# Kernel optimization log

Hardware: AMD Instinct MI355X
Metric: run time of the kernel (lower is better)

## Reference

```python
import math
import jax, jax.numpy as jnp
import numpy as np

B, S, H, M, E = 4, 4096, 1024, 1024, 16
CAPACITY_FACTOR = 2.0
ROUTE_SCALE = 1.0


def setup_inputs() -> dict:
    key = jax.random.key(0)
    ks = jax.random.split(key, 8)
    return {
        "hidden_states": jax.random.normal(ks[0], (B, S, H), dtype=jnp.float32),
        "hidden_states_unmodulated": jax.random.normal(ks[1], (B, S, H), dtype=jnp.float32),
        "timestep": jax.random.normal(ks[2], (B, H), dtype=jnp.float32),
        "gate_w": jax.random.normal(ks[3], (2 * H, E), dtype=jnp.float32) * 0.02,
        "gate_up_proj": jax.random.normal(ks[4], (E, H, 2 * M), dtype=jnp.float32) * 0.02,
        "down_proj": jax.random.normal(ks[5], (E, M, H), dtype=jnp.float32) * 0.02,
        "shared_gate_up_w": jax.random.normal(ks[6], (H, 2 * M), dtype=jnp.float32) * 0.02,
        "shared_down_w": jax.random.normal(ks[7], (M, H), dtype=jnp.float32) * 0.02,
    }


def reference(hidden_states, hidden_states_unmodulated, timestep, gate_w,
              gate_up_proj, down_proj, shared_gate_up_w, shared_down_w):
    b, s, h = hidden_states.shape
    e = gate_up_proj.shape[0]
    capacity = max(1, math.ceil(CAPACITY_FACTOR * s / e))  # static per shapes

    # --- router ---
    t = jnp.broadcast_to(timestep[:, None, :], (b, s, h))
    router_input = jnp.concatenate([t, hidden_states_unmodulated], axis=-1)  # [b,s,2h]
    logits = router_input @ gate_w                                           # [b,s,e]
    scores = jax.nn.sigmoid(logits.astype(jnp.float32)).astype(logits.dtype)
    affinity = jnp.swapaxes(scores, 1, 2)                                    # [b,e,s]

    # --- expert-choice top-k ---
    gating, top_idx = jax.lax.top_k(affinity, capacity)                      # [b,e,cap]
    offsets = (jnp.arange(b) * s)[:, None, None]
    gidx = jnp.swapaxes(offsets + top_idx, 0, 1).reshape(-1)                 # [e*b*cap]
    gflat = jnp.swapaxes(gating, 0, 1).reshape(-1)

    # normalize per-token scores over experts that picked the token
    sums = jnp.zeros(b * s, dtype=gflat.dtype).at[gidx].add(gflat)
    gflat = gflat / (sums[gidx] + 1e-12) * ROUTE_SCALE

    # --- dispatch + grouped SwiGLU experts ---
    x_flat = hidden_states.reshape(b * s, h)
    routed = x_flat[gidx].reshape(e, b * capacity, h)
    gu = jnp.einsum('eth,ehf->etf', routed, gate_up_proj)                    # [e,t,2m]
    g, u = jnp.split(gu, 2, axis=-1)
    expert_out = jnp.einsum('etm,emh->eth', jax.nn.silu(g) * u, down_proj)
    expert_out = expert_out.reshape(e * b * capacity, h)
    expert_out = (expert_out.astype(jnp.float32) *
                  gflat.astype(jnp.float32)[:, None]).astype(hidden_states.dtype)

    # --- shared expert (SwiGLUProj order: hidden * silu(gate)) ---
    hgu = hidden_states @ shared_gate_up_w                                   # [b,s,2m]
    hs_, hg = jnp.split(hgu, 2, axis=-1)
    shared = (hs_ * jax.nn.silu(hg)) @ shared_down_w                         # [b,s,h]

    # --- scatter combine ---
    out = shared.reshape(b * s, h).at[gidx].add(expert_out)
    return out.reshape(b, s, h)
```

## Files before the change

### kernel.cpp

```cpp
#include <hip/hip_runtime.h>
#include <math.h>

#define Bb 4
#define Ss 4096
#define Hh 1024
#define Mm 1024
#define Ee 16
#define CAPk 512

typedef unsigned short u16;
typedef __attribute__((ext_vector_type(8))) short short8;
typedef __attribute__((ext_vector_type(4))) float floatx4;
typedef __attribute__((ext_vector_type(4))) unsigned short ushort4v;

__device__ __forceinline__ float silu_f(float x) {
    return x / (1.0f + expf(-x));
}

__device__ __forceinline__ u16 f2b(float x) {
    union { float f; unsigned u; } v; v.f = x;
    unsigned r = (v.u + 0x7fffu + ((v.u >> 16) & 1u)) >> 16;
    return (u16)r;
}

__device__ __forceinline__ void gl_lds16(const void* g, void* l) {
    __builtin_amdgcn_global_load_lds((const __attribute__((address_space(1))) void*)g,
                                     (__attribute__((address_space(3))) void*)l, 16, 0, 0);
}


__global__ __launch_bounds__(256)
void conv_router(const float* __restrict__ hidden, u16* __restrict__ Xb,
                 const float* __restrict__ hsu,
                 const float* __restrict__ gate_w,
                 const float* __restrict__ timestep,
                 float* __restrict__ scores) {
    const int t = threadIdx.x;
    if (blockIdx.x >= 256) {
        int i = ((blockIdx.x - 256) * 256 + t) * 4;
        float4 v = *(const float4*)(hidden + i);
        ushort4v o = { f2b(v.x), f2b(v.y), f2b(v.z), f2b(v.w) };
        *(ushort4v*)(Xb + i) = o;
        return;
    }
    __shared__ float Xs[64 * 64];
    __shared__ float Gs[64 * 16];
    const int rbid = blockIdx.x;
    const int row0 = rbid * 64;
    const int b = row0 >> 12;
    const int wave = t >> 6, lane = t & 63;
    const int e0 = wave * 4;
    const float* gw2 = gate_w + (size_t)Hh * Ee;

    float tl0 = 0.f, tl1 = 0.f, tl2 = 0.f, tl3 = 0.f;
    {
        const float* tsrow = timestep + (size_t)b * Hh;
#pragma unroll
        for (int j = 0; j < 16; ++j) {
            int h = lane + 64 * j;
            float tv = tsrow[h];
            const float* gw = gate_w + (size_t)h * Ee + e0;
            tl0 += tv * gw[0]; tl1 += tv * gw[1]; tl2 += tv * gw[2]; tl3 += tv * gw[3];
        }
#pragma unroll
        for (int off = 32; off; off >>= 1) {
            tl0 += __shfl_xor(tl0, off); tl1 += __shfl_xor(tl1, off);
            tl2 += __shfl_xor(tl2, off); tl3 += __shfl_xor(tl3, off);
        }
    }

    float acc0 = 0.f, acc1 = 0.f, acc2 = 0.f, acc3 = 0.f;

    for (int k0 = 0; k0 < Hh; k0 += 64) {
        __syncthreads();
#pragma unroll
        for (int r = 0; r < 4; ++r) {
            int tok = r * 16 + (t >> 4);
            int cslot = t & 15;
            int g = cslot ^ (tok & 15);
            const float* src = hsu + (size_t)(row0 + tok) * Hh + k0 + g * 4;
            char* dst = (char*)Xs + r * 4096 + wave * 1024;
            gl_lds16(src, dst);
        }
        {
            const float* src = gw2 + (size_t)k0 * Ee + t * 4;
            char* dst = (char*)Gs + wave * 1024;
            gl_lds16(src, dst);
        }
        __syncthreads();
#pragma unroll
        for (int kk = 0; kk < 64; kk += 4) {
            int slot = (kk >> 2) ^ (lane & 15);
            float4 a = *(const float4*)&Xs[lane * 64 + slot * 4];
            float4 g0 = *(const float4*)&Gs[(kk + 0) * Ee + e0];
            float4 g1 = *(const float4*)&Gs[(kk + 1) * Ee + e0];
            float4 g2 = *(const float4*)&Gs[(kk + 2) * Ee + e0];
            float4 g3 = *(const float4*)&Gs[(kk + 3) * Ee + e0];
            acc0 += a.x * g0.x; acc0 += a.y * g1.x; acc0 += a.z * g2.x; acc0 += a.w * g3.x;
            acc1 += a.x * g0.y; acc1 += a.y * g1.y; acc1 += a.z * g2.y; acc1 += a.w * g3.y;
            acc2 += a.x * g0.z; acc2 += a.y * g1.z; acc2 += a.z * g2.z; acc2 += a.w * g3.z;
            acc3 += a.x * g0.w; acc3 += a.y * g1.w; acc3 += a.z * g2.w; acc3 += a.w * g3.w;
        }
    }
    const int s = (row0 + lane) & (Ss - 1);
    float l0 = acc0 + tl0;
    float l1 = acc1 + tl1;
    float l2 = acc2 + tl2;
    float l3 = acc3 + tl3;
    scores[((size_t)(b * Ee + e0 + 0)) * Ss + s] = 1.f / (1.f + expf(-l0));
    scores[((size_t)(b * Ee + e0 + 1)) * Ss + s] = 1.f / (1.f + expf(-l1));
    scores[((size_t)(b * Ee + e0 + 2)) * Ss + s] = 1.f / (1.f + expf(-l2));
    scores[((size_t)(b * Ee + e0 + 3)) * Ss + s] = 1.f / (1.f + expf(-l3));
}

__global__ __launch_bounds__(1024)
void topk_kernel(const float* __restrict__ scores,
                 int* __restrict__ rank) {
    const int be = blockIdx.x;
    const float* sc = scores + (size_t)be * Ss;
    int* rk = rank + (size_t)be * Ss;
    const int t = threadIdx.x;
    const int lane = t & 63, w = t >> 6;
    __shared__ unsigned hist[256];
    __shared__ unsigned wtot[16];
    __shared__ unsigned sh_prefix;
    __shared__ int sh_need;
    __shared__ unsigned cnt_gt;

#pragma unroll
    for (int i = 0; i < 4; ++i) rk[t * 4 + i] = -1;

    unsigned vu[4];
#pragma unroll
    for (int i = 0; i < 4; ++i) vu[i] = __float_as_uint(sc[t * 4 + i]);

    unsigned prefix = 0;
    int need = CAPk;
    for (int pass = 0; pass < 4; ++pass) {
        const int shift = 24 - 8 * pass;
        if (t < 256) hist[t] = 0;
        __syncthreads();
#pragma unroll
        for (int i = 0; i < 4; ++i) {
            unsigned u = vu[i];
            bool ok = (pass == 0) || ((u >> (shift + 8)) == prefix);
            if (ok) atomicAdd(&hist[(u >> shift) & 255u], 1u);
        }
        __syncthreads();
        unsigned hval = (t < 256) ? hist[t] : 0u;
        unsigned s = hval;
#pragma unroll
        for (int d = 1; d < 64; d <<= 1) {
            unsigned o = __shfl_down(s, d);
            if (lane + d < 64) s += o;
        }
        if (lane == 0 && w < 4) wtot[w] = s;
        __syncthreads();
        if (t < 256) {
#pragma unroll
            for (int w2 = 0; w2 < 4; ++w2)
                if (w2 > w) s += wtot[w2];
            unsigned Snext = s - hval;
            if (s >= (unsigned)need && Snext < (unsigned)need) {
                sh_prefix = (prefix << 8) | (unsigned)t;
                sh_need = need - (int)Snext;
            }
        }
        __syncthreads();
        prefix = sh_prefix;
        need = sh_need;
        __syncthreads();
    }
    const unsigned T = prefix;
    const int need_eq = need;
    const unsigned ngt = (unsigned)(CAPk - need_eq);

    int myeq = 0;
#pragma unroll
    for (int i = 0; i < 4; ++i) myeq += (vu[i] == T) ? 1 : 0;
    unsigned e = (unsigned)myeq;
#pragma unroll
    for (int d = 1; d < 64; d <<= 1) {
        unsigned o = __shfl_up(e, d);
        if (lane >= d) e += o;
    }
    if (lane == 63) wtot[w] = e;
    if (t == 0) cnt_gt = 0;
    __syncthreads();
    unsigned eqr = e - (unsigned)myeq;
#pragma unroll
    for (int w2 = 0; w2 < 16; ++w2)
        if (w2 < w) eqr += wtot[w2];
#pragma unroll
    for (int i = 0; i < 4; ++i) {
        unsigned u = vu[i];
        int s = t * 4 + i;
        if (u > T) {
            unsigned slot = atomicAdd(&cnt_gt, 1u);
            rk[s] = (int)slot;
        } else if (u == T) {
            if ((int)eqr < need_eq) {
                rk[s] = (int)(ngt + eqr);
            }
            eqr++;
        }
    }
}

__global__ __launch_bounds__(256)
void route_build(const float* __restrict__ scores, const int* __restrict__ rank,
                 int* __restrict__ slot_token, float* __restrict__ slot_w,
                 int* __restrict__ cnt, int* __restrict__ inv) {
    const int token = blockIdx.x * 256 + threadIdx.x;
    const int b = token >> 12, s = token & (Ss - 1);
    int rr[16];
    float gg[16];
    float sum = 0.f;
#pragma unroll
    for (int e = 0; e < 16; ++e) {
        size_t idx = (size_t)(b * Ee + e) * Ss + s;
        int r = rank[idx];
        rr[e] = r;
        float g = (r >= 0) ? scores[idx] : 0.f;
        gg[e] = g;
        sum += g;
    }
    int pos = 0;
#pragma unroll
    for (int e = 0; e < 16; ++e) {
        if (rr[e] >= 0) {
            float wv = gg[e] / (sum + 1e-12f);
            int o = (e * Bb + b) * CAPk + rr[e];
            slot_token[o] = token;
            slot_w[o] = wv;
            inv[token * 16 + pos] = o;
            ++pos;
        }
    }
    cnt[token] = pos;
}

__global__ __launch_bounds__(256)
void combine_kernel(const int* __restrict__ cnt, const int* __restrict__ inv,
                    const float* __restrict__ eo, float* __restrict__ out) {
    const int token = blockIdx.x;
    const int k = cnt[token];
    if (k == 0) return;
    const int col = threadIdx.x * 4;
    const size_t rowoff = (size_t)token * 1024 + col;
    float4 acc = *(const float4*)(out + rowoff);
    for (int j = 0; j < k; ++j) {
        int slot = inv[token * 16 + j];
        float4 v = *(const float4*)(eo + (size_t)slot * 1024 + col);
        acc.x += v.x; acc.y += v.y; acc.z += v.z; acc.w += v.w;
    }
    *(float4*)(out + rowoff) = acc;
}


__device__ __forceinline__ void tpose_body(const float* __restrict__ Ws, u16* __restrict__ Wd,
                                           int N, int n0, int k0, float tile[64][65], int t) {
    int lr = t >> 4, lc = (t & 15) * 4;
#pragma unroll
    for (int i = 0; i < 4; ++i) {
        float4 v = *(const float4*)&Ws[(size_t)(k0 + lr + i * 16) * N + n0 + lc];
        tile[lr + i * 16][lc + 0] = v.x;
        tile[lr + i * 16][lc + 1] = v.y;
        tile[lr + i * 16][lc + 2] = v.z;
        tile[lr + i * 16][lc + 3] = v.w;
    }
    __syncthreads();
    int on = t >> 2;
    int ok0 = (t & 3) * 16;
    u16 buf[16];
#pragma unroll
    for (int j = 0; j < 16; ++j) buf[j] = f2b(tile[ok0 + j][on]);
    u16* dp = &Wd[(size_t)(n0 + on) * 1024 + k0 + ok0];
    *(short8*)(dp) = *(short8*)&buf[0];
    *(short8*)(dp + 8) = *(short8*)&buf[8];
}

__global__ __launch_bounds__(256)
void transpose_bf16(const float* __restrict__ W, u16* __restrict__ Wt,
                    int N, size_t zsrc, size_t zdst) {
    __shared__ float tile[64][65];
    int n0 = blockIdx.x * 64, k0 = blockIdx.y * 64, z = blockIdx.z;
    tpose_body(W + (size_t)z * zsrc, Wt + (size_t)z * zdst, N, n0, k0, tile, threadIdx.x);
}

__global__ __launch_bounds__(256)
void transpose_all(const float* __restrict__ gate_up, const float* __restrict__ down,
                   const float* __restrict__ sh_gu, const float* __restrict__ sh_dn,
                   u16* __restrict__ Wt1r, u16* __restrict__ Wt2r,
                   u16* __restrict__ Wt1s, u16* __restrict__ Wt2s) {
    __shared__ float tile[64][65];
    const int id = blockIdx.x;
    const float* Ws; u16* Wd; int N, n0, k0;
    if (id < 8192) {
        int z = id >> 9, r = id & 511;
        n0 = (r & 31) * 64; k0 = (r >> 5) * 64; N = 2048;
        Ws = gate_up + (size_t)z * 2097152; Wd = Wt1r + (size_t)z * 2097152;
    } else if (id < 12288) {
        int i2 = id - 8192; int z = i2 >> 8, r = i2 & 255;
        n0 = (r & 15) * 64; k0 = (r >> 4) * 64; N = 1024;
        Ws = down + (size_t)z * 1048576; Wd = Wt2r + (size_t)z * 1048576;
    } else if (id < 12800) {
        int r = id - 12288;
        n0 = (r & 31) * 64; k0 = (r >> 5) * 64; N = 2048;
        Ws = sh_gu; Wd = Wt1s;
    } else {
        int r = id - 12800;
        n0 = (r & 15) * 64; k0 = (r >> 4) * 64; N = 1024;
        Ws = sh_dn; Wd = Wt2s;
    }
    tpose_body(Ws, Wd, N, n0, k0, tile, threadIdx.x);
}


__device__ __forceinline__ void stage_tile512(const u16* __restrict__ grow, int k0,
                                              u16* lds, int t) {
#pragma unroll
    for (int r = 0; r < 2; ++r) {
        int ci = r * 512 + t;
        int m = ci >> 3;
        int c = (ci & 7) ^ (m & 7);
        const u16* src = grow + (size_t)m * 1024 + k0 + c * 8;
        u16* dst = lds + ((r * 8192 + (t >> 6) * 1024) >> 1);
        gl_lds16(src, dst);
    }
}

__device__ __forceinline__ void stage_rows512(const u16* __restrict__ A, const int* rid,
                                              int k0, u16* lds, int t) {
#pragma unroll
    for (int r = 0; r < 2; ++r) {
        int ci = r * 512 + t;
        int m = ci >> 3;
        int c = (ci & 7) ^ (m & 7);
        const u16* src = A + (size_t)rid[r] * 1024 + k0 + c * 8;
        u16* dst = lds + ((r * 8192 + (t >> 6) * 1024) >> 1);
        gl_lds16(src, dst);
    }
}

template <bool SILU_FIRST, bool GATHER>
__global__ __launch_bounds__(512, 4)
void gemm1_mfma(const u16* __restrict__ A, int a_row0, int zstride,
                const u16* __restrict__ W1t, u16* __restrict__ act,
                const int* __restrict__ slot_token, int e_base) {
    __shared__ u16 lA[128 * 64];
    __shared__ u16 lB1[128 * 64];
    __shared__ u16 lB2[128 * 64];
    const int t = threadIdx.x;
    const int n0 = blockIdx.x * 128;
    const int bm0 = blockIdx.y * 128;
    const int z = blockIdx.z;
    const int zb = z * zstride;
    const u16* B1row = W1t + ((size_t)z * 2048 + n0) * 1024;
    const u16* B2row = B1row + (size_t)1024 * 1024;
    const int lane = t & 63;
    const int wv = t >> 6;
    const int wm = wv & 1, wn = wv >> 1;
    const int quad = lane >> 4, l15 = lane & 15;

    int rid[2];
#pragma unroll
    for (int r = 0; r < 2; ++r) {
        int m = (t >> 3) + 64 * r;
        rid[r] = GATHER ? slot_token[(e_base + z) * (Bb * CAPk) + bm0 + m]
                        : (a_row0 + zb + bm0 + m);
    }

    floatx4 zero4 = {0.f, 0.f, 0.f, 0.f};
    floatx4 acc1[4][2], acc2[4][2];
#pragma unroll
    for (int i = 0; i < 4; ++i)
#pragma unroll
        for (int j = 0; j < 2; ++j) { acc1[i][j] = zero4; acc2[i][j] = zero4; }

    for (int k0 = 0; k0 < 1024; k0 += 64) {
        __syncthreads();
        stage_rows512(A, rid, k0, lA, t);
        stage_tile512(B1row, k0, lB1, t);
        stage_tile512(B2row, k0, lB2, t);
        __syncthreads();
#pragma unroll
        for (int kc = 0; kc < 2; ++kc) {
            short8 af[4], bf1[2], bf2[2];
#pragma unroll
            for (int mi = 0; mi < 4; ++mi) {
                int m = wm * 64 + mi * 16 + l15;
                int off = m * 64 + (((kc * 4 + quad) ^ (m & 7)) * 8);
                af[mi] = *(const short8*)&lA[off];
            }
#pragma unroll
            for (int ni = 0; ni < 2; ++ni) {
                int n = wn * 32 + ni * 16 + l15;
                int off = n * 64 + (((kc * 4 + quad) ^ (n & 7)) * 8);
                bf1[ni] = *(const short8*)&lB1[off];
                bf2[ni] = *(const short8*)&lB2[off];
            }
#pragma unroll
            for (int mi = 0; mi < 4; ++mi)
#pragma unroll
                for (int ni = 0; ni < 2; ++ni) {
                    acc1[mi][ni] = __builtin_amdgcn_mfma_f32_16x16x32_bf16(af[mi], bf1[ni], acc1[mi][ni], 0, 0, 0);
                    acc2[mi][ni] = __builtin_amdgcn_mfma_f32_16x16x32_bf16(af[mi], bf2[ni], acc2[mi][ni], 0, 0, 0);
                }
        }
    }
#pragma unroll
    for (int mi = 0; mi < 4; ++mi)
#pragma unroll
        for (int ni = 0; ni < 2; ++ni)
#pragma unroll
            for (int r = 0; r < 4; ++r) {
                int m = wm * 64 + mi * 16 + quad * 4 + r;
                int n = wn * 32 + ni * 16 + l15;
                float c1 = acc1[mi][ni][r], c2 = acc2[mi][ni][r];
                float v = SILU_FIRST ? silu_f(c1) * c2 : c1 * silu_f(c2);
                act[(size_t)(zb + bm0 + m) * 1024 + n0 + n] = f2b(v);
            }
}

template <int MODE>
__global__ __launch_bounds__(512, 4)
void gemm2_mfma(const u16* __restrict__ A, int zstride,
                const u16* __restrict__ W2t,
                const int* __restrict__ slot_token, const float* __restrict__ slot_w,
                float* __restrict__ out, int out_row0, int e_base) {
    __shared__ u16 lA[128 * 64];
    __shared__ u16 lB[128 * 64];
    __shared__ int s_tok[(MODE == 1) ? 128 : 1];
    __shared__ float s_w[(MODE == 1 || MODE == 2) ? 128 : 1];
    const int t = threadIdx.x;
    const int n0 = blockIdx.x * 128;
    const int bm0 = blockIdx.y * 128;
    const int z = blockIdx.z;
    const int zb = z * zstride;
    const u16* Arow = A + (size_t)(zb + bm0) * 1024;
    const u16* Brow = W2t + ((size_t)z * 1024 + n0) * 1024;
    const int lane = t & 63;
    const int wv = t >> 6;
    const int wm = wv & 1, wn = wv >> 1;
    const int quad = lane >> 4, l15 = lane & 15;

    if ((MODE == 1 || MODE == 2) && t < 128) {
        int gi = (e_base + z) * (Bb * CAPk) + bm0 + t;
        if (MODE == 1) s_tok[t] = slot_token[gi];
        s_w[t] = slot_w[gi];
    }

    floatx4 zero4 = {0.f, 0.f, 0.f, 0.f};
    floatx4 acc[4][2];
#pragma unroll
    for (int i = 0; i < 4; ++i)
#pragma unroll
        for (int j = 0; j < 2; ++j) acc[i][j] = zero4;

    for (int k0 = 0; k0 < 1024; k0 += 64) {
        __syncthreads();
        stage_tile512(Arow, k0, lA, t);
        stage_tile512(Brow, k0, lB, t);
        __syncthreads();
#pragma unroll
        for (int kc = 0; kc < 2; ++kc) {
            short8 af[4], bf[2];
#pragma unroll
            for (int mi = 0; mi < 4; ++mi) {
                int m = wm * 64 + mi * 16 + l15;
                int off = m * 64 + (((kc * 4 + quad) ^ (m & 7)) * 8);
                af[mi] = *(const short8*)&lA[off];
            }
#pragma unroll
            for (int ni = 0; ni < 2; ++ni) {
                int n = wn * 32 + ni * 16 + l15;
                int off = n * 64 + (((kc * 4 + quad) ^ (n & 7)) * 8);
                bf[ni] = *(const short8*)&lB[off];
            }
#pragma unroll
            for (int mi = 0; mi < 4; ++mi)
#pragma unroll
                for (int ni = 0; ni < 2; ++ni)
                    acc[mi][ni] = __builtin_amdgcn_mfma_f32_16x16x32_bf16(af[mi], bf[ni], acc[mi][ni], 0, 0, 0);
        }
    }
#pragma unroll
    for (int mi = 0; mi < 4; ++mi)
#pragma unroll
        for (int ni = 0; ni < 2; ++ni)
#pragma unroll
            for (int r = 0; r < 4; ++r) {
                int m = wm * 64 + mi * 16 + quad * 4 + r;
                int n = wn * 32 + ni * 16 + l15;
                float c = acc[mi][ni][r];
                if (MODE == 1) {
                    atomicAdd(&out[(size_t)s_tok[m] * 1024 + n0 + n], c * s_w[m]);
                } else if (MODE == 2) {
                    out[((size_t)((e_base + z) * (Bb * CAPk) + bm0 + m)) * 1024 + n0 + n] = c * s_w[m];
                } else {
                    out[(size_t)(out_row0 + bm0 + m) * 1024 + n0 + n] = c;
                }
            }
}


extern "C" void kernel_launch(void* const* d_in, const int* in_sizes, int n_in,
                              void* d_out, int out_size, void* d_ws, size_t ws_size,
                              hipStream_t stream) {
    const float* hidden   = (const float*)d_in[0];
    const float* hsu      = (const float*)d_in[1];
    const float* timestep = (const float*)d_in[2];
    const float* gate_w   = (const float*)d_in[3];
    const float* gate_up  = (const float*)d_in[4];
    const float* down     = (const float*)d_in[5];
    const float* sh_gu    = (const float*)d_in[6];
    const float* sh_dn    = (const float*)d_in[7];
    float* out = (float*)d_out;

    char* p = (char*)d_ws;
    auto alloc = [&](size_t bytes) { char* r = p; p += (bytes + 255) & ~(size_t)255; return r; };
    float* scores    = (float*)alloc((size_t)Bb * Ee * Ss * 4);
    int*   rank      = (int*)  alloc((size_t)Bb * Ee * Ss * 4);
    int*   slot_token= (int*)  alloc((size_t)Ee * Bb * CAPk * 4);
    float* slot_w    = (float*)alloc((size_t)Ee * Bb * CAPk * 4);
    int*   cnt       = (int*)  alloc((size_t)Bb * Ss * 4);
    int*   inv       = (int*)  alloc((size_t)Bb * Ss * 16 * 4);
    u16*   Xb        = (u16*)  alloc((size_t)16384 * 1024 * 2);
    char* phase = p;
    long long avail = (long long)((char*)d_ws + ws_size - phase);
    if (avail < 0) avail = 0;

    const long long eo_bytes     = (long long)32768 * 1024 * 4;
    const long long per_e        = ((long long)2048 * 1024 + 1024 * 1024 +
                                    (long long)2048 * 1024) * 2;
    const long long shared_fixed = ((long long)2048 * 1024 + 1024 * 1024) * 2;
    const long long fast_need    = ((long long)16 * 2048 * 1024 +
                                    (long long)16 * 1024 * 1024 +
                                    (long long)16 * 2048 * 1024 +
                                    (long long)2048 * 1024 +
                                    (long long)1024 * 1024) * 2;

    conv_router<<<16384 + (Bb * Ss) / 64, 256, 0, stream>>>(hidden, Xb, hsu, gate_w,
                                                            timestep, scores);
    topk_kernel<<<Bb * Ee, 1024, 0, stream>>>(scores, rank);
    route_build<<<(Bb * Ss) / 256, 256, 0, stream>>>(scores, rank, slot_token, slot_w,
                                                     cnt, inv);

    bool use_eo = (avail >= eo_bytes + (per_e > (shared_fixed + (long long)128 * 2048)
                                        ? per_e : (shared_fixed + (long long)128 * 2048)));
    bool fast   = use_eo && (avail - eo_bytes >= fast_need);

    if (fast) {
        float* eo = (float*)phase;
        char* ph2 = phase + eo_bytes;
        u16* Wt1r = (u16*)ph2;
        u16* Wt2r = Wt1r + (size_t)16 * 2048 * 1024;
        u16* actR = Wt2r + (size_t)16 * 1024 * 1024;
        u16* Wt1s = actR + (size_t)16 * 2048 * 1024;
        u16* Wt2s = Wt1s + (size_t)2048 * 1024;
        u16* actS = Wt1r;

        transpose_all<<<13056, 256, 0, stream>>>(gate_up, down, sh_gu, sh_dn,
                                                 Wt1r, Wt2r, Wt1s, Wt2s);
        gemm1_mfma<true, true><<<dim3(8, 16, 8), 512, 0, stream>>>(
            Xb, 0, 2048, Wt1r, actR, slot_token, 0);
        gemm1_mfma<true, true><<<dim3(8, 16, 8), 512, 0, stream>>>(
            Xb, 0, 2048, Wt1r + (size_t)8 * 2048 * 1024,
            actR + (size_t)8 * 2048 * 1024, slot_token, 8);
        gemm2_mfma<2><<<dim3(8, 16, 16), 512, 0, stream>>>(
            actR, 2048, Wt2r, slot_token, slot_w, eo, 0, 0);
        gemm1_mfma<false, false><<<dim3(8, 128, 1), 512, 0, stream>>>(
            Xb, 0, 0, Wt1s, actS, nullptr, 0);
        gemm2_mfma<0><<<dim3(8, 128, 1), 512, 0, stream>>>(
            actS, 0, Wt2s, nullptr, nullptr, out, 0, 0);
        combine_kernel<<<Bb * Ss, 256, 0, stream>>>(cnt, inv, eo, out);
    } else if (use_eo) {
        float* eo = (float*)phase;
        char* ph2 = phase + eo_bytes;
        long long avail2 = avail - eo_bytes;
        {
            int g = (int)(avail2 / per_e);
            if (g < 1) g = 1;
            if (g > Ee) g = Ee;
            u16* Wt1r = (u16*)ph2;
            u16* Wt2r = Wt1r + (size_t)g * 2048 * 1024;
            u16* actR = Wt2r + (size_t)g * 1024 * 1024;
            for (int e0 = 0; e0 < Ee; e0 += g) {
                int cg = Ee - e0; if (cg > g) cg = g;
                transpose_bf16<<<dim3(32, 16, cg), 256, 0, stream>>>(
                    gate_up + (size_t)e0 * 2097152, Wt1r, 2048, 2097152, 2097152);
                transpose_bf16<<<dim3(16, 16, cg), 256, 0, stream>>>(
                    down + (size_t)e0 * 1048576, Wt2r, 1024, 1048576, 1048576);
                gemm1_mfma<true, true><<<dim3(8, 16, cg), 512, 0, stream>>>(
                    Xb, 0, 2048, Wt1r, actR, slot_token, e0);
                gemm2_mfma<2><<<dim3(8, 16, cg), 512, 0, stream>>>(
                    actR, 2048, Wt2r, slot_token, slot_w, eo, 0, e0);
            }
        }
        {
            u16* Wt1s = (u16*)ph2;
            u16* Wt2s = Wt1s + (size_t)2048 * 1024;
            u16* actS = Wt2s + (size_t)1024 * 1024;
            long long room = (avail2 - shared_fixed) / 2048;
            room &= ~127LL;
            int R = (int)(room > 16384 ? 16384 : room);
            if (R < 128) R = 128;
            transpose_bf16<<<dim3(32, 16, 1), 256, 0, stream>>>(sh_gu, Wt1s, 2048, 0, 0);
            transpose_bf16<<<dim3(16, 16, 1), 256, 0, stream>>>(sh_dn, Wt2s, 1024, 0, 0);
            for (int r0 = 0; r0 < Bb * Ss; r0 += R) {
                int cur = Bb * Ss - r0; if (cur > R) cur = R;
                gemm1_mfma<false, false><<<dim3(8, cur / 128, 1), 512, 0, stream>>>(
                    Xb, r0, 0, Wt1s, actS, nullptr, 0);
                gemm2_mfma<0><<<dim3(8, cur / 128, 1), 512, 0, stream>>>(
                    actS, 0, Wt2s, nullptr, nullptr, out, r0, 0);
            }
        }
        combine_kernel<<<Bb * Ss, 256, 0, stream>>>(cnt, inv, eo, out);
    } else {
        {
            u16* Wt1s = (u16*)phase;
            u16* Wt2s = Wt1s + (size_t)2048 * 1024;
            u16* actS = Wt2s + (size_t)1024 * 1024;
            long long room = (avail - shared_fixed) / 2048;
            room &= ~127LL;
            int R = (int)(room > 16384 ? 16384 : room);
            if (R < 128) R = 128;
            transpose_bf16<<<dim3(32, 16, 1), 256, 0, stream>>>(sh_gu, Wt1s, 2048, 0, 0);
            transpose_bf16<<<dim3(16, 16, 1), 256, 0, stream>>>(sh_dn, Wt2s, 1024, 0, 0);
            for (int r0 = 0; r0 < Bb * Ss; r0 += R) {
                int cur = Bb * Ss - r0; if (cur > R) cur = R;
                gemm1_mfma<false, false><<<dim3(8, cur / 128, 1), 512, 0, stream>>>(
                    Xb, r0, 0, Wt1s, actS, nullptr, 0);
                gemm2_mfma<0><<<dim3(8, cur / 128, 1), 512, 0, stream>>>(
                    actS, 0, Wt2s, nullptr, nullptr, out, r0, 0);
            }
        }
        {
            int g = (int)(avail / per_e);
            if (g < 1) g = 1;
            if (g > Ee) g = Ee;
            u16* Wt1r = (u16*)phase;
            u16* Wt2r = Wt1r + (size_t)g * 2048 * 1024;
            u16* actR = Wt2r + (size_t)g * 1024 * 1024;
            for (int e0 = 0; e0 < Ee; e0 += g) {
                int cg = Ee - e0; if (cg > g) cg = g;
                transpose_bf16<<<dim3(32, 16, cg), 256, 0, stream>>>(
                    gate_up + (size_t)e0 * 2097152, Wt1r, 2048, 2097152, 2097152);
                transpose_bf16<<<dim3(16, 16, cg), 256, 0, stream>>>(
                    down + (size_t)e0 * 1048576, Wt2r, 1024, 1048576, 1048576);
                gemm1_mfma<true, true><<<dim3(8, 16, cg), 512, 0, stream>>>(
                    Xb, 0, 2048, Wt1r, actR, slot_token, e0);
                gemm2_mfma<1><<<dim3(8, 16, cg), 512, 0, stream>>>(
                    actR, 2048, Wt2r, slot_token, slot_w, out, 0, e0);
            }
        }
    }
}
```

Baseline: 792.1 us.

## Remap GEMM tiles onto flat 1D grid with chunked launches for weight locality

```diff
diff --git a/kernel.cpp b/kernel.cpp
--- a/kernel.cpp
+++ b/kernel.cpp
@@ -345,6 +345,175 @@
 
 template <bool SILU_FIRST, bool GATHER>
 __global__ __launch_bounds__(512, 4)
+void gemm1_flat(const u16* __restrict__ A,
+                const u16* __restrict__ W1t, u16* __restrict__ act,
+                const int* __restrict__ slot_token, int p0, int p1) {
+    __shared__ u16 lA[128 * 64];
+    __shared__ u16 lB1[128 * 64];
+    __shared__ u16 lB2[128 * 64];
+    const int t = threadIdx.x;
+    const int L = blockIdx.x;
+    const int x = L & 7, j = L >> 3;
+    int z = 0, bm0, n0;
+    if (GATHER) {
+        if (p1 == 8) { z = p0 + x; bm0 = (j >> 3) << 7; }
+        else         { z = p0 + (x >> 1); bm0 = (((x & 1) << 3) + (j >> 3)) << 7; }
+    } else {
+        bm0 = (p0 + x * (p1 >> 3) + (j >> 3)) << 7;
+    }
+    n0 = (j & 7) << 7;
+    const int out_base = (GATHER ? z * 2048 : 0) + bm0;
+    const u16* B1row = W1t + ((size_t)(GATHER ? z * 2048 : 0) + n0) * 1024;
+    const u16* B2row = B1row + (size_t)1024 * 1024;
+    const int lane = t & 63;
+    const int wv = t >> 6;
+    const int wm = wv & 1, wn = wv >> 1;
+    const int quad = lane >> 4, l15 = lane & 15;
+
+    int rid[2];
+#pragma unroll
+    for (int r = 0; r < 2; ++r) {
+        int m = (t >> 3) + 64 * r;
+        rid[r] = GATHER ? slot_token[z * (Bb * CAPk) + bm0 + m] : (bm0 + m);
+    }
+
+    floatx4 zero4 = {0.f, 0.f, 0.f, 0.f};
+    floatx4 acc1[4][2], acc2[4][2];
+#pragma unroll
+    for (int i = 0; i < 4; ++i)
+#pragma unroll
+        for (int j2 = 0; j2 < 2; ++j2) { acc1[i][j2] = zero4; acc2[i][j2] = zero4; }
+
+    for (int k0 = 0; k0 < 1024; k0 += 64) {
+        __syncthreads();
+        stage_rows512(A, rid, k0, lA, t);
+        stage_tile512(B1row, k0, lB1, t);
+        stage_tile512(B2row, k0, lB2, t);
+        __syncthreads();
+#pragma unroll
+        for (int kc = 0; kc < 2; ++kc) {
+            short8 af[4], bf1[2], bf2[2];
+#pragma unroll
+            for (int mi = 0; mi < 4; ++mi) {
+                int m = wm * 64 + mi * 16 + l15;
+                int off = m * 64 + (((kc * 4 + quad) ^ (m & 7)) * 8);
+                af[mi] = *(const short8*)&lA[off];
+            }
+#pragma unroll
+            for (int ni = 0; ni < 2; ++ni) {
+                int n = wn * 32 + ni * 16 + l15;
+                int off = n * 64 + (((kc * 4 + quad) ^ (n & 7)) * 8);
+                bf1[ni] = *(const short8*)&lB1[off];
+                bf2[ni] = *(const short8*)&lB2[off];
+            }
+#pragma unroll
+            for (int mi = 0; mi < 4; ++mi)
+#pragma unroll
+                for (int ni = 0; ni < 2; ++ni) {
+                    acc1[mi][ni] = __builtin_amdgcn_mfma_f32_16x16x32_bf16(af[mi], bf1[ni], acc1[mi][ni], 0, 0, 0);
+                    acc2[mi][ni] = __builtin_amdgcn_mfma_f32_16x16x32_bf16(af[mi], bf2[ni], acc2[mi][ni], 0, 0, 0);
+                }
+        }
+    }
+#pragma unroll
+    for (int mi = 0; mi < 4; ++mi)
+#pragma unroll
+        for (int ni = 0; ni < 2; ++ni)
+#pragma unroll
+            for (int r = 0; r < 4; ++r) {
+                int m = wm * 64 + mi * 16 + quad * 4 + r;
+                int n = wn * 32 + ni * 16 + l15;
+                float c1 = acc1[mi][ni][r], c2 = acc2[mi][ni][r];
+                float v = SILU_FIRST ? silu_f(c1) * c2 : c1 * silu_f(c2);
+                act[(size_t)(out_base + m) * 1024 + n0 + n] = f2b(v);
+            }
+}
+
+template <int MODE>
+__global__ __launch_bounds__(512, 4)
+void gemm2_flat(const u16* __restrict__ A,
+                const u16* __restrict__ W2t, const float* __restrict__ slot_w,
+                float* __restrict__ outp, int p0, int p1) {
+    __shared__ u16 lA[128 * 64];
+    __shared__ u16 lB[128 * 64];
+    __shared__ float s_w[(MODE == 2) ? 128 : 1];
+    const int t = threadIdx.x;
+    const int L = blockIdx.x;
+    const int x = L & 7, j = L >> 3;
+    int z = 0, bm0, n0;
+    if (MODE == 2) {
+        if (p1 == 8) { z = p0 + x; bm0 = (j >> 3) << 7; }
+        else         { z = p0 + (x >> 1); bm0 = (((x & 1) << 3) + (j >> 3)) << 7; }
+    } else {
+        bm0 = (p0 + x * (p1 >> 3) + (j >> 3)) << 7;
+    }
+    n0 = (j & 7) << 7;
+    const int row_base = (MODE == 2 ? z * 2048 : 0) + bm0;
+    const u16* Arow = A + (size_t)row_base * 1024;
+    const u16* Brow = W2t + ((size_t)(MODE == 2 ? z * 1024 : 0) + n0) * 1024;
+    const int lane = t & 63;
+    const int wv = t >> 6;
+    const int wm = wv & 1, wn = wv >> 1;
+    const int quad = lane >> 4, l15 = lane & 15;
+
+    if (MODE == 2 && t < 128) {
+        s_w[t] = slot_w[row_base + t];
+    }
+
+    floatx4 zero4 = {0.f, 0.f, 0.f, 0.f};
+    floatx4 acc[4][2];
+#pragma unroll
+    for (int i = 0; i < 4; ++i)
+#pragma unroll
+        for (int j2 = 0; j2 < 2; ++j2) acc[i][j2] = zero4;
+
+    for (int k0 = 0; k0 < 1024; k0 += 64) {
+        __syncthreads();
+        stage_tile512(Arow, k0, lA, t);
+        stage_tile512(Brow, k0, lB, t);
+        __syncthreads();
+#pragma unroll
+        for (int kc = 0; kc < 2; ++kc) {
+            short8 af[4], bf[2];
+#pragma unroll
+            for (int mi = 0; mi < 4; ++mi) {
+                int m = wm * 64 + mi * 16 + l15;
+                int off = m * 64 + (((kc * 4 + quad) ^ (m & 7)) * 8);
+                af[mi] = *(const short8*)&lA[off];
+            }
+#pragma unroll
+            for (int ni = 0; ni < 2; ++ni) {
+                int n = wn * 32 + ni * 16 + l15;
+                int off = n * 64 + (((kc * 4 + quad) ^ (n & 7)) * 8);
+                bf[ni] = *(const short8*)&lB[off];
+            }
+#pragma unroll
+            for (int mi = 0; mi < 4; ++mi)
+#pragma unroll
+                for (int ni = 0; ni < 2; ++ni)
+                    acc[mi][ni] = __builtin_amdgcn_mfma_f32_16x16x32_bf16(af[mi], bf[ni], acc[mi][ni], 0, 0, 0);
+        }
+    }
+#pragma unroll
+    for (int mi = 0; mi < 4; ++mi)
+#pragma unroll
+        for (int ni = 0; ni < 2; ++ni)
+#pragma unroll
+            for (int r = 0; r < 4; ++r) {
+                int m = wm * 64 + mi * 16 + quad * 4 + r;
+                int n = wn * 32 + ni * 16 + l15;
+                float c = acc[mi][ni][r];
+                if (MODE == 2) {
+                    outp[(size_t)(row_base + m) * 1024 + n0 + n] = c * s_w[m];
+                } else {
+                    outp[(size_t)(row_base + m) * 1024 + n0 + n] = c;
+                }
+            }
+}
+
+
+template <bool SILU_FIRST, bool GATHER>
+__global__ __launch_bounds__(512, 4)
 void gemm1_mfma(const u16* __restrict__ A, int a_row0, int zstride,
                 const u16* __restrict__ W1t, u16* __restrict__ act,
                 const int* __restrict__ slot_token, int e_base) {
@@ -563,17 +732,17 @@
 
         transpose_all<<<13056, 256, 0, stream>>>(gate_up, down, sh_gu, sh_dn,
                                                  Wt1r, Wt2r, Wt1s, Wt2s);
-        gemm1_mfma<true, true><<<dim3(8, 16, 8), 512, 0, stream>>>(
-            Xb, 0, 2048, Wt1r, actR, slot_token, 0);
-        gemm1_mfma<true, true><<<dim3(8, 16, 8), 512, 0, stream>>>(
-            Xb, 0, 2048, Wt1r + (size_t)8 * 2048 * 1024,
-            actR + (size_t)8 * 2048 * 1024, slot_token, 8);
-        gemm2_mfma<2><<<dim3(8, 16, 16), 512, 0, stream>>>(
-            actR, 2048, Wt2r, slot_token, slot_w, eo, 0, 0);
-        gemm1_mfma<false, false><<<dim3(8, 128, 1), 512, 0, stream>>>(
-            Xb, 0, 0, Wt1s, actS, nullptr, 0);
-        gemm2_mfma<0><<<dim3(8, 128, 1), 512, 0, stream>>>(
-            actS, 0, Wt2s, nullptr, nullptr, out, 0, 0);
+        for (int e0 = 0; e0 < 16; e0 += 4)
+            gemm1_flat<true, true><<<512, 512, 0, stream>>>(
+                Xb, Wt1r, actR, slot_token, e0, 4);
+        gemm2_flat<2><<<1024, 512, 0, stream>>>(actR, Wt2r, slot_w, eo, 0, 8);
+        gemm2_flat<2><<<1024, 512, 0, stream>>>(actR, Wt2r, slot_w, eo, 8, 8);
+        gemm1_flat<false, false><<<512, 512, 0, stream>>>(
+            Xb, Wt1s, actS, nullptr, 0, 64);
+        gemm1_flat<false, false><<<512, 512, 0, stream>>>(
+            Xb, Wt1s, actS, nullptr, 64, 64);
+        gemm2_flat<0><<<512, 512, 0, stream>>>(actS, Wt2s, nullptr, out, 0, 64);
+        gemm2_flat<0><<<512, 512, 0, stream>>>(actS, Wt2s, nullptr, out, 64, 64);
         combine_kernel<<<Bb * Ss, 256, 0, stream>>>(cnt, inv, eo, out);
     } else if (use_eo) {
         float* eo = (float*)phase;
```

New measurement: 796.6 us. About the same (+0.6%).
